# Kernel optimization log

Hardware: AMD Instinct MI355X
Metric: run time of the kernel (lower is better)

Reference implementation:

```python
import jax, jax.numpy as jnp
import numpy as np

SQ, B, NH, HD = 2048, 2, 16, 128  # seq, batch, heads, head_dim


def setup_inputs() -> dict:
    key = jax.random.key(0)
    kq, kk, kv = jax.random.split(key, 3)
    shape = (SQ, B, NH, HD)
    return {
        "query": jax.random.normal(kq, shape, dtype=jnp.float32),
        "key": jax.random.normal(kk, shape, dtype=jnp.float32),
        "value": jax.random.normal(kv, shape, dtype=jnp.float32),
        "attention_mask": jnp.ones((B, 1, SQ, SQ), dtype=bool),
    }


def reference(query, key, value, attention_mask):
    # query/key/value: [s, b, n, h]
    sq, b, n_heads, hn = query.shape
    norm_factor = jnp.sqrt(jnp.asarray(hn, query.dtype))
    # QK^T -> [b, n, sq, sk]
    scores = jnp.einsum("sbnh,tbnh->bnst", query, key) / norm_factor
    probs = jax.nn.softmax(scores, axis=-1, where=attention_mask)
    # PV -> [s, b, n, h]  (dropout is identity at p=0.0 / eval)
    context = jnp.einsum("bnst,tbnh->sbnh", probs, value)
    return context.reshape(sq, b, n_heads * hn)
```

## Files before the change

kernel.cpp:

```cpp
#include <hip/hip_runtime.h>
#include <hip/hip_bf16.h>
#include <math.h>


#define SQ 2048
#define NBH 32
#define HD 128
#define RSTRIDE 4096
#define BQ 128
#define BK 32
#define NKT (SQ / BK)
#define TILE_E (BK * HD)
#define HELEMS (SQ * HD)
#define SCALE_LOG2E 0.12751879523499918f
#define THR_LOG2 8.0f

typedef __attribute__((ext_vector_type(4)))  float f32x4;
typedef __attribute__((ext_vector_type(16))) float f32x16;
typedef __attribute__((ext_vector_type(4)))  short s16x4;
typedef __attribute__((ext_vector_type(8)))  short s16x8;

#define MFMA32(a, b, c) __builtin_amdgcn_mfma_f32_32x32x16_bf16((a), (b), (c), 0, 0, 0)

__device__ __forceinline__ short f2bf(float f) {
    __hip_bfloat16 h = __float2bfloat16(f);
    return __builtin_bit_cast(short, h);
}
__device__ __forceinline__ unsigned pk2(float lo, float hi) {
    unsigned r;
    asm("v_cvt_pk_bf16_f32 %0, %1, %2" : "=v"(r) : "v"(lo), "v"(hi));
    return r;
}

__device__ __forceinline__ void stage16(const void* g, void* l) {
    __builtin_amdgcn_global_load_lds(
        (const __attribute__((address_space(1))) unsigned int*)g,
        (__attribute__((address_space(3))) unsigned int*)l, 16, 0, 0);
}

__global__ __launch_bounds__(256) void prep_qk(const float* __restrict__ Q,
                                               const float* __restrict__ K,
                                               short* __restrict__ wq,
                                               short* __restrict__ wk) {
    const int id = blockIdx.x * 256 + threadIdx.x;
    const int bh = id >> 15;
    const int s  = (id >> 4) & 2047;
    const int c  = id & 15;
    const size_t outoff = (size_t)bh * HELEMS + (size_t)s * HD + c * 8;
    {
        const float* src = Q + (size_t)s * RSTRIDE + bh * HD + c * 8;
        f32x4 a = *(const f32x4*)src;
        f32x4 b = *(const f32x4*)(src + 4);
        s16x8 f;
        #pragma unroll
        for (int j = 0; j < 4; ++j) {
            f[j]     = f2bf(a[j] * SCALE_LOG2E);
            f[4 + j] = f2bf(b[j] * SCALE_LOG2E);
        }
        *(s16x8*)(wq + outoff) = f;
    }
    {
        const int cl = c ^ (s & 7);
        const float* src = K + (size_t)s * RSTRIDE + bh * HD + cl * 8;
        f32x4 a = *(const f32x4*)src;
        f32x4 b = *(const f32x4*)(src + 4);
        s16x8 f;
        #pragma unroll
        for (int j = 0; j < 4; ++j) { f[j] = f2bf(a[j]); f[4 + j] = f2bf(b[j]); }
        *(s16x8*)(wk + outoff) = f;
    }
}

__global__ __launch_bounds__(256) void prep_v(const float* __restrict__ V,
                                              short* __restrict__ wv) {
    const int kt = blockIdx.x;
    const int bh = blockIdx.y;
    const int tid = threadIdx.x;
    __shared__ short L[32 * 132];

    #pragma unroll
    for (int it = 0; it < 4; ++it) {
        const int id = it * 256 + tid;
        const int row = id >> 5, p = id & 31;
        f32x4 a = *(const f32x4*)(V + (size_t)(kt * BK + row) * RSTRIDE + bh * HD + p * 4);
        s16x4 f;
        #pragma unroll
        for (int j = 0; j < 4; ++j) f[j] = f2bf(a[j]);
        *(s16x4*)&L[row * 132 + p * 4] = f;
    }
    __syncthreads();
    #pragma unroll
    for (int it = 0; it < 2; ++it) {
        const int id = it * 256 + tid;
        const int dim = id >> 2, pc = id & 3;
        const int klb = (pc ^ ((dim >> 1) & 3)) * 8;
        s16x8 f;
        #pragma unroll
        for (int j = 0; j < 8; ++j) f[j] = L[(klb + j) * 132 + dim];
        *(s16x8*)(wv + (size_t)bh * HELEMS + (size_t)kt * TILE_E + dim * BK + pc * 8) = f;
    }
}

__global__ __launch_bounds__(256) void fa_fwd5(const short* __restrict__ Qb,
                                               const short* __restrict__ Kb,
                                               const short* __restrict__ Vb,
                                               float* __restrict__ O) {
    const int id  = blockIdx.x;
    const int xcd = id & 7;
    const int s8  = id >> 3;
    const int bh  = xcd * 4 + (s8 >> 4);
    const int qt  = s8 & 15;

    const int tid  = threadIdx.x;
    const int w    = tid >> 6;
    const int lane = tid & 63;
    const int l32  = lane & 31;
    const int hi   = lane >> 5;

    __shared__ short Kt[2][TILE_E];
    __shared__ short Vt[2][TILE_E];

    const size_t hb = (size_t)bh * HELEMS;
    const int q = qt * BQ + w * 32 + l32;
    const int vsw = (l32 >> 1) & 3;

    s16x8 qf[8];
    {
        const short* qp = Qb + hb + (size_t)q * HD + hi * 8;
        #pragma unroll
        for (int kd = 0; kd < 8; ++kd) qf[kd] = *(const s16x8*)(qp + kd * 16);
    }

    f32x16 acc[4];
    #pragma unroll
    for (int db = 0; db < 4; ++db)
        #pragma unroll
        for (int i = 0; i < 16; ++i) acc[db][i] = 0.0f;
    float m = -INFINITY, l = 0.0f;

    auto STAGE = [&](int kt, int buf) {
        const size_t toff = hb + (size_t)kt * TILE_E;
        const short* kg = Kb + toff + (2 * w) * 512 + lane * 8;
        stage16(kg,       &Kt[buf][(2 * w) * 512 + lane * 8]);
        stage16(kg + 512, &Kt[buf][(2 * w + 1) * 512 + lane * 8]);
        const short* vg = Vb + toff + (2 * w) * 512 + lane * 8;
        stage16(vg,       &Vt[buf][(2 * w) * 512 + lane * 8]);
        stage16(vg + 512, &Vt[buf][(2 * w + 1) * 512 + lane * 8]);
    };

    STAGE(0, 0);
    __syncthreads();
    int buf = 0;

    #pragma unroll 1
    for (int kt = 0; kt < NKT; ++kt) {
        f32x16 sc;
        #pragma unroll
        for (int i = 0; i < 16; ++i) sc[i] = 0.0f;
        __builtin_amdgcn_s_setprio(1);
        #pragma unroll
        for (int kd = 0; kd < 8; ++kd) {
            const int elem = l32 * HD + (((kd << 1) | hi) ^ (l32 & 7)) * 8;
            s16x8 kf = *(const s16x8*)&Kt[buf][elem];
            sc = MFMA32(kf, qf[kd], sc);
        }
        __builtin_amdgcn_s_setprio(0);

        if (kt + 1 < NKT) STAGE(kt + 1, buf ^ 1);

        float u0 = fmaxf(sc[0], sc[1]),   u1 = fmaxf(sc[2], sc[3]);
        float u2 = fmaxf(sc[4], sc[5]),   u3 = fmaxf(sc[6], sc[7]);
        float u4 = fmaxf(sc[8], sc[9]),   u5 = fmaxf(sc[10], sc[11]);
        float u6 = fmaxf(sc[12], sc[13]), u7 = fmaxf(sc[14], sc[15]);
        u0 = fmaxf(u0, u1); u2 = fmaxf(u2, u3); u4 = fmaxf(u4, u5); u6 = fmaxf(u6, u7);
        const float mt = fmaxf(fmaxf(u0, u2), fmaxf(u4, u6));
        const float m0 = fmaxf(mt, __shfl_xor(mt, 32, 64));
        const bool need = (m0 > m + THR_LOG2);
        const float mn = need ? fmaxf(m, m0) : m;
        if (__any(need)) {
            const float alpha = exp2f(m - mn);
            m = mn;
            l *= alpha;
            #pragma unroll
            for (int db = 0; db < 4; ++db) acc[db] *= alpha;
        }

        float lsp = 0.0f;
        #pragma unroll
        for (int ks = 0; ks < 2; ++ks) {
            float p0 = exp2f(sc[8 * ks + 0] - m), p1 = exp2f(sc[8 * ks + 1] - m);
            float p2 = exp2f(sc[8 * ks + 2] - m), p3 = exp2f(sc[8 * ks + 3] - m);
            float p4 = exp2f(sc[8 * ks + 4] - m), p5 = exp2f(sc[8 * ks + 5] - m);
            float p6 = exp2f(sc[8 * ks + 6] - m), p7 = exp2f(sc[8 * ks + 7] - m);
            lsp += ((p0 + p1) + (p2 + p3)) + ((p4 + p5) + (p6 + p7));
            unsigned a0 = pk2(p0, p1), a1 = pk2(p2, p3);
            unsigned b0 = pk2(p4, p5), b1 = pk2(p6, p7);
            s16x8 pa;
#if __has_builtin(__builtin_amdgcn_permlane32_swap)
            {
                auto r0 = __builtin_amdgcn_permlane32_swap(a0, b0, false, false);
                auto r1 = __builtin_amdgcn_permlane32_swap(a1, b1, false, false);
                union { unsigned u[4]; s16x8 v; } P;
                P.u[0] = r0[0]; P.u[1] = r1[0]; P.u[2] = r0[1]; P.u[3] = r1[1];
                pa = P.v;
            }
#else
            {
                const unsigned s0 = __shfl_xor(hi ? a0 : b0, 32, 64);
                const unsigned s1 = __shfl_xor(hi ? a1 : b1, 32, 64);
                union { unsigned u[4]; s16x8 v; } P;
                P.u[0] = hi ? s0 : a0; P.u[1] = hi ? s1 : a1;
                P.u[2] = hi ? b0 : s0; P.u[3] = hi ? b1 : s1;
                pa = P.v;
            }
#endif
            const int pc = ((ks << 1) | hi) ^ vsw;
            __builtin_amdgcn_s_setprio(1);
            #pragma unroll
            for (int db = 0; db < 4; ++db) {
                const int elem = (db * 32 + l32) * BK + pc * 8;
                s16x8 vf = *(const s16x8*)&Vt[buf][elem];
                acc[db] = MFMA32(vf, pa, acc[db]);
            }
            __builtin_amdgcn_s_setprio(0);
        }
        l += lsp;

        __syncthreads();
        buf ^= 1;
    }

    const float lf = l + __shfl_xor(l, 32, 64);
    const float invl = 1.0f / lf;
    float* op = O + (size_t)q * RSTRIDE + bh * HD;
    #pragma unroll
    for (int db = 0; db < 4; ++db)
        #pragma unroll
        for (int j = 0; j < 4; ++j) {
            f32x4 o;
            #pragma unroll
            for (int r = 0; r < 4; ++r) o[r] = acc[db][4 * j + r] * invl;
            *(f32x4*)(op + db * 32 + j * 8 + hi * 4) = o;
        }
}

__global__ __launch_bounds__(256) void fa_fwd_legacy(const float* __restrict__ Q,
                                                     const float* __restrict__ K,
                                                     const float* __restrict__ V,
                                                     float* __restrict__ O) {
    const int qt   = blockIdx.x;
    const int bh   = blockIdx.y;
    const int tid  = threadIdx.x;
    const int w    = tid >> 6;
    const int lane = tid & 63;
    const int l16  = lane & 15;
    const int lg   = lane >> 4;

    __shared__ short Kt[64 * HD];
    __shared__ short Vt[HD * 64];
    __shared__ short Pl[4][16 * 72];

    const int headoff = bh * HD;
    s16x8 qf[4];
    {
        const int qrow = qt * 64 + w * 16 + l16;
        const float* qp = Q + (size_t)qrow * RSTRIDE + headoff + lg * 8;
        #pragma unroll
        for (int ks = 0; ks < 4; ++ks) {
            f32x4 a = *(const f32x4*)(qp + ks * 32);
            f32x4 b = *(const f32x4*)(qp + ks * 32 + 4);
            s16x8 f;
            #pragma unroll
            for (int j = 0; j < 4; ++j) {
                f[j]     = f2bf(a[j] * SCALE_LOG2E);
                f[4 + j] = f2bf(b[j] * SCALE_LOG2E);
            }
            qf[ks] = f;
        }
    }
    f32x4 acc[8];
    #pragma unroll
    for (int i = 0; i < 8; ++i)
        #pragma unroll
        for (int j = 0; j < 4; ++j) acc[i][j] = 0.0f;
    float mrow[4], lrow[4];
    #pragma unroll
    for (int r = 0; r < 4; ++r) { mrow[r] = -INFINITY; lrow[r] = 0.0f; }
    const int skey = tid >> 2;
    const int sdc  = tid & 3;
    const int va   = tid >> 3;
    const int vdc  = tid & 7;

    for (int kt = 0; kt < SQ / 64; ++kt) {
        __syncthreads();
        {
            const float* kp = K + (size_t)(kt * 64 + skey) * RSTRIDE + headoff;
            #pragma unroll
            for (int c = 0; c < 4; ++c) {
                const int d0 = c * 32 + sdc * 8;
                f32x4 a = *(const f32x4*)(kp + d0);
                f32x4 b = *(const f32x4*)(kp + d0 + 4);
                s16x8 f;
                #pragma unroll
                for (int j = 0; j < 4; ++j) { f[j] = f2bf(a[j]); f[4 + j] = f2bf(b[j]); }
                const int elem = (skey * HD + d0) ^ ((skey & 7) << 3);
                *(s16x8*)&Kt[elem] = f;
            }
        }
        {
            const float* vp0 = V + (size_t)(kt * 64 + va * 2) * RSTRIDE + headoff;
            const float* vp1 = vp0 + RSTRIDE;
            #pragma unroll
            for (int c = 0; c < 4; ++c) {
                const int d0 = c * 32 + vdc * 4;
                f32x4 a0 = *(const f32x4*)(vp0 + d0);
                f32x4 a1 = *(const f32x4*)(vp1 + d0);
                #pragma unroll
                for (int j = 0; j < 4; ++j) {
                    const int dim = d0 + j;
                    const int s = (dim ^ (dim >> 3)) & 7;
                    const int elem = (dim * 64 + va * 2) ^ (s << 3);
                    union { short u[2]; int i; } pr;
                    pr.u[0] = f2bf(a0[j]);
                    pr.u[1] = f2bf(a1[j]);
                    *(int*)&Vt[elem] = pr.i;
                }
            }
        }
        __syncthreads();
        f32x4 sc[4];
        #pragma unroll
        for (int t = 0; t < 4; ++t) {
            #pragma unroll
            for (int j = 0; j < 4; ++j) sc[t][j] = 0.0f;
            const int key = t * 16 + l16;
            #pragma unroll
            for (int ks = 0; ks < 4; ++ks) {
                const int elem = (key * HD + ks * 32 + lg * 8) ^ ((key & 7) << 3);
                s16x8 kf = *(const s16x8*)&Kt[elem];
                sc[t] = __builtin_amdgcn_mfma_f32_16x16x32_bf16(qf[ks], kf, sc[t], 0, 0, 0);
            }
        }
        float alpha[4];
        #pragma unroll
        for (int r = 0; r < 4; ++r) {
            float m0 = fmaxf(fmaxf(sc[0][r], sc[1][r]), fmaxf(sc[2][r], sc[3][r]));
            #pragma unroll
            for (int d = 1; d < 16; d <<= 1) m0 = fmaxf(m0, __shfl_xor(m0, d, 64));
            const float mnew = fmaxf(mrow[r], m0);
            alpha[r] = exp2f(mrow[r] - mnew);
            mrow[r] = mnew;
        }
        float rsum[4] = {0.f, 0.f, 0.f, 0.f};
        #pragma unroll
        for (int t = 0; t < 4; ++t)
            #pragma unroll
            for (int r = 0; r < 4; ++r) {
                const float p = exp2f(sc[t][r] - mrow[r]);
                sc[t][r] = p;
                rsum[r] += p;
            }
        #pragma unroll
        for (int r = 0; r < 4; ++r) {
            #pragma unroll
            for (int d = 1; d < 16; d <<= 1) rsum[r] += __shfl_xor(rsum[r], d, 64);
            lrow[r] = lrow[r] * alpha[r] + rsum[r];
        }
        #pragma unroll
        for (int ct = 0; ct < 8; ++ct)
            #pragma unroll
            for (int r = 0; r < 4; ++r) acc[ct][r] *= alpha[r];
        #pragma unroll
        for (int t = 0; t < 4; ++t)
            #pragma unroll
            for (int r = 0; r < 4; ++r)
                Pl[w][(lg * 4 + r) * 72 + t * 16 + l16] = f2bf(sc[t][r]);
        s16x8 pf[2];
        #pragma unroll
        for (int ks = 0; ks < 2; ++ks)
            pf[ks] = *(const s16x8*)&Pl[w][l16 * 72 + ks * 32 + lg * 8];
        #pragma unroll
        for (int ct = 0; ct < 8; ++ct) {
            const int dim = ct * 16 + l16;
            const int s = (dim ^ (dim >> 3)) & 7;
            #pragma unroll
            for (int ks = 0; ks < 2; ++ks) {
                const int elem = (dim * 64 + ks * 32 + lg * 8) ^ (s << 3);
                s16x8 vf = *(const s16x8*)&Vt[elem];
                acc[ct] = __builtin_amdgcn_mfma_f32_16x16x32_bf16(pf[ks], vf, acc[ct], 0, 0, 0);
            }
        }
    }
    float inv_l[4];
    #pragma unroll
    for (int r = 0; r < 4; ++r) inv_l[r] = 1.0f / lrow[r];
    const int orow0 = qt * 64 + w * 16;
    #pragma unroll
    for (int ct = 0; ct < 8; ++ct) {
        const int col = ct * 16 + l16;
        #pragma unroll
        for (int r = 0; r < 4; ++r) {
            const int row = orow0 + lg * 4 + r;
            O[(size_t)row * RSTRIDE + headoff + col] = acc[ct][r] * inv_l[r];
        }
    }
}

extern "C" void kernel_launch(void* const* d_in, const int* in_sizes, int n_in,
                              void* d_out, int out_size, void* d_ws, size_t ws_size,
                              hipStream_t stream) {
    const float* Q = (const float*)d_in[0];
    const float* K = (const float*)d_in[1];
    const float* V = (const float*)d_in[2];
    float* O = (float*)d_out;

    const size_t need = (size_t)3 * NBH * HELEMS * sizeof(short);
    if (ws_size >= need) {
        short* wq = (short*)d_ws;
        short* wk = wq + (size_t)NBH * HELEMS;
        short* wv = wk + (size_t)NBH * HELEMS;
        prep_qk<<<4096, 256, 0, stream>>>(Q, K, wq, wk);
        prep_v<<<dim3(NKT, NBH), 256, 0, stream>>>(V, wv);
        fa_fwd5<<<(SQ / BQ) * NBH, 256, 0, stream>>>(wq, wk, wv, O);
    } else {
        fa_fwd_legacy<<<dim3(SQ / 64, NBH), 256, 0, stream>>>(Q, K, V, O);
    }
}
```

Before: 141.5 us.

## Split KV sequence across two blocks with 512-thread tiles and merge pass

Query tiles grow to 256 rows handled by 8 waves, with K staged by four waves and V by the other four. The key sequence is split in two (split-K flash attention). Each half writes an unnormalized partial output plus max and sum to workspace, and a new merge kernel combines them. The aim is to keep the grid at 512 blocks despite the larger tiles, raising per-block K/V reuse while keeping occupancy. The cost is extra fp32 partial-output traffic and one more kernel launch.

```diff
diff --git a/kernel.cpp b/kernel.cpp
--- a/kernel.cpp
+++ b/kernel.cpp
@@ -7,11 +7,11 @@
 #define NBH 32
 #define HD 128
 #define RSTRIDE 4096
-#define BQ 128
+#define BQ 256
 #define BK 32
-#define NKT (SQ / BK)
 #define TILE_E (BK * HD)
 #define HELEMS (SQ * HD)
+#define OELEMS ((size_t)SQ * RSTRIDE)
 #define SCALE_LOG2E 0.12751879523499918f
 #define THR_LOG2 8.0f
 
@@ -101,15 +101,19 @@
     }
 }
 
-__global__ __launch_bounds__(256) void fa_fwd5(const short* __restrict__ Qb,
-                                               const short* __restrict__ Kb,
-                                               const short* __restrict__ Vb,
-                                               float* __restrict__ O) {
+template <int G>
+__global__ __launch_bounds__(512, 4) void fa_fwd6(const short* __restrict__ Qb,
+                                                  const short* __restrict__ Kb,
+                                                  const short* __restrict__ Vb,
+                                                  float* __restrict__ Out,
+                                                  float* __restrict__ ml) {
     const int id  = blockIdx.x;
     const int xcd = id & 7;
     const int s8  = id >> 3;
-    const int bh  = xcd * 4 + (s8 >> 4);
-    const int qt  = s8 & 15;
+    const int bh  = xcd * 4 + s8 / (8 * G);
+    const int r   = s8 % (8 * G);
+    const int qt  = r / G;
+    const int g   = r % G;
 
     const int tid  = threadIdx.x;
     const int w    = tid >> 6;
@@ -140,20 +144,28 @@
 
     auto STAGE = [&](int kt, int buf) {
         const size_t toff = hb + (size_t)kt * TILE_E;
-        const short* kg = Kb + toff + (2 * w) * 512 + lane * 8;
-        stage16(kg,       &Kt[buf][(2 * w) * 512 + lane * 8]);
-        stage16(kg + 512, &Kt[buf][(2 * w + 1) * 512 + lane * 8]);
-        const short* vg = Vb + toff + (2 * w) * 512 + lane * 8;
-        stage16(vg,       &Vt[buf][(2 * w) * 512 + lane * 8]);
-        stage16(vg + 512, &Vt[buf][(2 * w + 1) * 512 + lane * 8]);
+        if (w < 4) {
+            const short* kg = Kb + toff + w * 1024 + lane * 8;
+            stage16(kg,       &Kt[buf][w * 1024 + lane * 8]);
+            stage16(kg + 512, &Kt[buf][w * 1024 + lane * 8 + 512]);
+        } else {
+            const int w4 = w - 4;
+            const short* vg = Vb + toff + w4 * 1024 + lane * 8;
+            stage16(vg,       &Vt[buf][w4 * 1024 + lane * 8]);
+            stage16(vg + 512, &Vt[buf][w4 * 1024 + lane * 8 + 512]);
+        }
     };
 
-    STAGE(0, 0);
+    const int kt0 = g * (SQ / G / BK);
+    const int nkt = SQ / G / BK;
+
+    STAGE(kt0, 0);
     __syncthreads();
     int buf = 0;
 
     #pragma unroll 1
-    for (int kt = 0; kt < NKT; ++kt) {
+    for (int t = 0; t < nkt; ++t) {
+        const int kt = kt0 + t;
         f32x16 sc;
         #pragma unroll
         for (int i = 0; i < 16; ++i) sc[i] = 0.0f;
@@ -166,7 +178,7 @@
         }
         __builtin_amdgcn_s_setprio(0);
 
-        if (kt + 1 < NKT) STAGE(kt + 1, buf ^ 1);
+        if (t + 1 < nkt) STAGE(kt + 1, buf ^ 1);
 
         float u0 = fmaxf(sc[0], sc[1]),   u1 = fmaxf(sc[2], sc[3]);
         float u2 = fmaxf(sc[4], sc[5]),   u3 = fmaxf(sc[6], sc[7]);
@@ -231,17 +243,56 @@
     }
 
     const float lf = l + __shfl_xor(l, 32, 64);
-    const float invl = 1.0f / lf;
-    float* op = O + (size_t)q * RSTRIDE + bh * HD;
-    #pragma unroll
-    for (int db = 0; db < 4; ++db)
-        #pragma unroll
-        for (int j = 0; j < 4; ++j) {
-            f32x4 o;
-            #pragma unroll
-            for (int r = 0; r < 4; ++r) o[r] = acc[db][4 * j + r] * invl;
-            *(f32x4*)(op + db * 32 + j * 8 + hi * 4) = o;
-        }
+    if (G == 1) {
+        const float invl = 1.0f / lf;
+        float* op = Out + (size_t)q * RSTRIDE + bh * HD;
+        #pragma unroll
+        for (int db = 0; db < 4; ++db)
+            #pragma unroll
+            for (int j = 0; j < 4; ++j) {
+                f32x4 o;
+                #pragma unroll
+                for (int rr = 0; rr < 4; ++rr) o[rr] = acc[db][4 * j + rr] * invl;
+                *(f32x4*)(op + db * 32 + j * 8 + hi * 4) = o;
+            }
+    } else {
+        float* op = Out + (size_t)g * OELEMS + (size_t)q * RSTRIDE + bh * HD;
+        #pragma unroll
+        for (int db = 0; db < 4; ++db)
+            #pragma unroll
+            for (int j = 0; j < 4; ++j) {
+                f32x4 o;
+                #pragma unroll
+                for (int rr = 0; rr < 4; ++rr) o[rr] = acc[db][4 * j + rr];
+                *(f32x4*)(op + db * 32 + j * 8 + hi * 4) = o;
+            }
+        if (hi == 0) {
+            float* mlp = ml + ((size_t)g * SQ * NBH + (size_t)q * NBH + bh) * 2;
+            mlp[0] = m;
+            mlp[1] = lf;
+        }
+    }
+}
+
+__global__ __launch_bounds__(256) void fa_merge(const float* __restrict__ Op,
+                                                const float* __restrict__ ml,
+                                                float* __restrict__ O) {
+    const size_t idx = (size_t)blockIdx.x * 256 + threadIdx.x;
+    const size_t e = idx * 4;
+    const int q  = (int)(e >> 12);
+    const int bh = ((int)e >> 7) & 31;
+    const size_t mloff = ((size_t)q * NBH + bh) * 2;
+    const float m0 = ml[mloff], l0 = ml[mloff + 1];
+    const float m1 = ml[(size_t)SQ * NBH * 2 + mloff], l1 = ml[(size_t)SQ * NBH * 2 + mloff + 1];
+    const float M  = fmaxf(m0, m1);
+    const float w0 = exp2f(m0 - M), w1 = exp2f(m1 - M);
+    const float invL = 1.0f / (w0 * l0 + w1 * l1);
+    f32x4 o0 = *(const f32x4*)(Op + e);
+    f32x4 o1 = *(const f32x4*)(Op + OELEMS + e);
+    f32x4 o;
+    #pragma unroll
+    for (int j = 0; j < 4; ++j) o[j] = (o0[j] * w0 + o1[j] * w1) * invL;
+    *(f32x4*)(O + e) = o;
 }
 
 __global__ __launch_bounds__(256) void fa_fwd_legacy(const float* __restrict__ Q,
@@ -414,14 +465,23 @@
     const float* V = (const float*)d_in[2];
     float* O = (float*)d_out;
 
-    const size_t need = (size_t)3 * NBH * HELEMS * sizeof(short);
-    if (ws_size >= need) {
+    const size_t need_bf  = (size_t)3 * NBH * HELEMS * sizeof(short);
+    const size_t need_g2  = need_bf + 2 * OELEMS * sizeof(float)
+                          + (size_t)2 * SQ * NBH * 2 * sizeof(float);
+    if (ws_size >= need_bf) {
         short* wq = (short*)d_ws;
         short* wk = wq + (size_t)NBH * HELEMS;
         short* wv = wk + (size_t)NBH * HELEMS;
         prep_qk<<<4096, 256, 0, stream>>>(Q, K, wq, wk);
-        prep_v<<<dim3(NKT, NBH), 256, 0, stream>>>(V, wv);
-        fa_fwd5<<<(SQ / BQ) * NBH, 256, 0, stream>>>(wq, wk, wv, O);
+        prep_v<<<dim3(SQ / BK, NBH), 256, 0, stream>>>(V, wv);
+        if (ws_size >= need_g2) {
+            float* Op = (float*)((char*)d_ws + need_bf);
+            float* ml = Op + 2 * OELEMS;
+            fa_fwd6<2><<<512, 512, 0, stream>>>(wq, wk, wv, Op, ml);
+            fa_merge<<<(int)(OELEMS / 4 / 256), 256, 0, stream>>>(Op, ml, O);
+        } else {
+            fa_fwd6<1><<<256, 512, 0, stream>>>(wq, wk, wv, O, nullptr);
+        }
     } else {
         fa_fwd_legacy<<<dim3(SQ / 64, NBH), 256, 0, stream>>>(Q, K, V, O);
     }
```

Result: slower. 214.4 us (+51.6%).
